# Optimization experiments

Hardware: AMD Instinct MI355X
Metric: run time of the kernel (lower is better)

The kernel has to match this reference:

```python
import jax, jax.numpy as jnp
import numpy as np

PS = 7  # window size
HEADS = 8


def setup_inputs() -> dict:
    key = jax.random.key(0)
    ks = jax.random.split(key, 5)
    b, C, H, W = 2, 384, 224, 224
    x = jax.random.normal(ks[0], (b, C, H, W), dtype=jnp.float32)
    # Conv2d(dim, 3*dim, k=1, bias=False) -> weight [3C, C]
    qkv_w = jax.random.normal(ks[1], (3 * C, C), dtype=jnp.float32) * (1.0 / np.sqrt(C))
    # depthwise Conv2d(3*dim, 3*dim, k=3, groups=3*dim) -> weight [3C, 1, 3, 3]
    dw_w = jax.random.normal(ks[2], (3 * C, 1, 3, 3), dtype=jnp.float32) * (1.0 / 3.0)
    # temperature parameter, initialized to ones like the module
    temperature = jnp.ones((HEADS, 1, 1), dtype=jnp.float32)
    # Conv2d(dim, dim, k=1, bias=False) -> weight [C, C]
    proj_w = jax.random.normal(ks[3], (C, C), dtype=jnp.float32) * (1.0 / np.sqrt(C))
    return {"x": x, "qkv_w": qkv_w, "dw_w": dw_w, "temperature": temperature, "proj_w": proj_w}


def _l2norm(t):
    n = jnp.sqrt(jnp.sum(t * t, axis=-1, keepdims=True))
    return t / jnp.maximum(n, 1e-12)  # matches F.normalize semantics


def reference(x, qkv_w, dw_w, temperature, proj_w):
    b, C, H, W = x.shape
    heads, ps = HEADS, PS
    d = C // heads
    nh, nw = H // ps, W // ps

    # 1x1 conv qkv projection (pointwise -> einsum)
    qkv = jnp.einsum('bchw,oc->bohw', x, qkv_w)
    # depthwise 3x3 conv, padding=1
    qkv = jax.lax.conv_general_dilated(
        qkv, dw_w, window_strides=(1, 1), padding='SAME',
        feature_group_count=3 * C, dimension_numbers=('NCHW', 'OIHW', 'NCHW'))
    q, k, v = jnp.split(qkv, 3, axis=1)

    def to_win(t):
        # b (head d) (nh ps) (nw ps) -> b (nh nw) head d (ps ps)
        t = t.reshape(b, heads, d, nh, ps, nw, ps)
        t = t.transpose(0, 3, 5, 1, 2, 4, 6)
        return t.reshape(b, nh * nw, heads, d, ps * ps)

    q, k, v = to_win(q), to_win(k), to_win(v)
    q = _l2norm(q)
    k = _l2norm(k)

    # channel-transposed attention: d x d scores per window
    attn = jnp.einsum('bwhds,bwhes->bwhde', q, k) * temperature
    attn = jax.nn.softmax(attn, axis=-1)
    out = jnp.einsum('bwhde,bwhes->bwhds', attn, v)

    # inverse rearrange: b (nh nw) head d (ps ps) -> b (head d) (nh ps) (nw ps)
    out = out.reshape(b, nh, nw, heads, d, ps, ps)
    out = out.transpose(0, 3, 4, 1, 5, 2, 6).reshape(b, C, H, W)

    return jnp.einsum('bchw,oc->bohw', out, proj_w)
```

## Files before the change

kernel.cpp:

```cpp
#include <hip/hip_runtime.h>


#define NB     2
#define CC     384
#define C3     1152
#define HH     224
#define WW2    224
#define HW     50176
#define NHEADS 8
#define DD     48
#define PSZ    7
#define NWINS  1024
#define SS     49
#define SSP    56
#define WSR    (NWINS*SSP)

typedef unsigned int  u32;
typedef unsigned short u16;
typedef __bf16 bf16x8 __attribute__((ext_vector_type(8)));
typedef float  f32x4  __attribute__((ext_vector_type(4)));

__device__ __forceinline__ u16 f2bf(float f){
  union { __bf16 h; u16 u; } v; v.h = (__bf16)f; return v.u;
}
__device__ __forceinline__ float bf2f(u16 h){
  union { u32 u; float f; } v; v.u = ((u32)h) << 16;
  return v.f;
}
__device__ __forceinline__ float u16lo(u32 u){
  union { u32 u; float f; } v; v.u = u << 16; return v.f;
}
__device__ __forceinline__ float u16hi(u32 u){
  union { u32 u; float f; } v; v.u = u & 0xffff0000u; return v.f;
}

typedef __attribute__((address_space(3))) u32 as3_u32;
typedef __attribute__((address_space(1))) const u32 as1_u32;
__device__ __forceinline__ void gld16(const void* g, void* l){
  __builtin_amdgcn_global_load_lds((as1_u32*)(unsigned long long)(g),
                                   (as3_u32*)(u32)(unsigned long long)(l),
                                   16, 0, 0);
}

__device__ __forceinline__ int xcdswz(int bid, int cpx){
  return (bid & 7)*cpx + (bid >> 3);
}

__device__ __forceinline__ int swz(int row, int col){
  return row*64 + (col ^ ((row & 7) << 3));
}

__global__ void k_cvt(const float* __restrict__ qw, const float* __restrict__ pw,
                      u16* __restrict__ qwb, u16* __restrict__ pwb){
  int i = blockIdx.x * 256 + threadIdx.x;
  if (i < C3*CC) qwb[i] = f2bf(qw[i]);
  if (i < CC*CC) pwb[i] = f2bf(pw[i]);
}

__global__ void k_sentinel(float* __restrict__ out, int n){
  int i = blockIdx.x * 256 + threadIdx.x;
  if (i < n) out[i] = 12345.0f;
}

#define CPAD 386
__global__ __launch_bounds__(256) void k_trx(const float* __restrict__ x,
                                             u16* __restrict__ xt){
  const int pt = blockIdx.x, b = blockIdx.y, tid = threadIdx.x;
  __shared__ u16 t[64*CPAD];
  const float* xb = x + (size_t)b*CC*HW + pt*64;
  #pragma unroll
  for (int it=0; it<24; ++it){
    int i = tid + it*256;
    int c = i >> 4, p4 = (i & 15)*4;
    float4 v = *(const float4*)(xb + (size_t)c*HW + p4);
    t[(p4+0)*CPAD + c] = f2bf(v.x);
    t[(p4+1)*CPAD + c] = f2bf(v.y);
    t[(p4+2)*CPAD + c] = f2bf(v.z);
    t[(p4+3)*CPAD + c] = f2bf(v.w);
  }
  __syncthreads();
  u32* dst = (u32*)(xt + ((size_t)b*HW + (size_t)pt*64)*CC);
  #pragma unroll
  for (int it=0; it<48; ++it){
    int j = tid + it*256;
    int p = j / 192, c2 = j - p*192;
    dst[j] = *(const u32*)(t + p*CPAD + c2*2);
  }
}

template<int OUT_F32, int MT, int CPX>
__global__ __launch_bounds__(256) void k_gemm(const u16* __restrict__ A,
    const u16* __restrict__ B, void* __restrict__ Cdst){
  __shared__ __align__(16) u16 As0[128*64], Bs0[128*64];
  __shared__ __align__(16) u16 As1[128*64], Bs1[128*64];
  const int wg = xcdswz(blockIdx.x, CPX);
  const int m0 = (wg % MT) * 128;
  const int t1 = wg / MT;
  const int n0 = (t1 % 392) * 128;
  const int b  = t1 / 392;
  const int M  = MT * 128;
  const int tid = threadIdx.x, lane = tid & 63, wv = tid >> 6;
  const int wm = (wv & 1) * 64, wn = (wv >> 1) * 64;
  const int lr = lane & 15, lg = lane >> 4;
  const u16* Bb = B + (size_t)b*HW*CC;

  f32x4 acc[4][4];
  #pragma unroll
  for (int i=0;i<4;++i)
    #pragma unroll
    for (int j=0;j<4;++j) acc[i][j] = {0.f,0.f,0.f,0.f};

  const int srow[4] = { (tid+  0)>>3, (tid+256)>>3, (tid+512)>>3, (tid+768)>>3 };
  const int sc8  = tid & 7;

  #define STAGE(AD, BD, K0) {                                             \
    _Pragma("unroll")                                                     \
    for (int i=0;i<4;++i){                                                \
      int row = srow[i];                                                  \
      int csrc = sc8 ^ (row & 7);                                         \
      gld16(A  + (size_t)(m0+row)*CC + (K0) + csrc*8, AD + (i*256+tid)*8);\
      gld16(Bb + (size_t)(n0+row)*CC + (K0) + csrc*8, BD + (i*256+tid)*8);\
    } }

  #define COMPUTE(AD, BD) {                                               \
    _Pragma("unroll")                                                     \
    for (int ks=0; ks<2; ++ks){                                           \
      const int cp = (((ks*4 + lg) ^ (lr & 7)) << 3);                     \
      bf16x8 af[4], bfr[4];                                               \
      _Pragma("unroll")                                                   \
      for (int i=0;i<4;++i) af[i]  = *(const bf16x8*)(AD + (wm + i*16 + lr)*64 + cp); \
      _Pragma("unroll")                                                   \
      for (int j=0;j<4;++j) bfr[j] = *(const bf16x8*)(BD + (wn + j*16 + lr)*64 + cp); \
      _Pragma("unroll")                                                   \
      for (int i=0;i<4;++i)                                               \
        _Pragma("unroll")                                                 \
        for (int j=0;j<4;++j)                                             \
          acc[i][j] = __builtin_amdgcn_mfma_f32_16x16x32_bf16(af[i], bfr[j], acc[i][j], 0, 0, 0); \
    } }

  STAGE(As0, Bs0, 0)
  __syncthreads();
  #pragma unroll
  for (int kk2=0; kk2<3; ++kk2){
    const int k0 = kk2*128;
    if (kk2*2+1 < 6) STAGE(As1, Bs1, k0+64)
    COMPUTE(As0, Bs0)
    __syncthreads();
    if (kk2*2+2 < 6) STAGE(As0, Bs0, k0+128)
    COMPUTE(As1, Bs1)
    __syncthreads();
  }
  #undef STAGE
  #undef COMPUTE

  #pragma unroll
  for (int i=0;i<4;++i){
    #pragma unroll
    for (int j=0;j<4;++j){
      const int row = m0 + wm + i*16 + lg*4;
      const int col = n0 + wn + j*16 + lr;
      if (OUT_F32){
        float* Cp = (float*)Cdst + (size_t)b*M*HW;
        #pragma unroll
        for (int r=0;r<4;++r) Cp[(size_t)(row+r)*HW + col] = acc[i][j][r];
      } else {
        u16* Cp = (u16*)Cdst + (size_t)b*M*HW;
        #pragma unroll
        for (int r=0;r<4;++r) Cp[(size_t)(row+r)*HW + col] = f2bf(acc[i][j][r]);
      }
    }
  }
}

#define DWL 240
__global__ __launch_bounds__(128) void k_dw(const u16* __restrict__ qkv,
    const float* __restrict__ dww, u16* __restrict__ qkv2){
  const int wg = xcdswz(blockIdx.x, 2304);
  const int wy = wg & 31;
  const int t1 = wg >> 5;
  const int o0 = (t1 % 288) * 4;
  const int b  = t1 / 288;
  const int tid = threadIdx.x;
  __shared__ __align__(16) u16 lin[4*9*DWL];

  const int y0 = wy*PSZ - 1;

  if (tid < 72){
    int ch = tid/18, rem = tid%18, r = rem>>1;
    lin[ch*9*DWL + r*DWL + ((rem&1) ? 232 : 7)] = 0;
  }

  #pragma unroll
  for (int it=0; it<8; ++it){
    int i = tid + it*128;
    if (i < 1008){
      int ch = i / 252, rem = i - ch*252;
      int r = rem / 28, c16 = rem - r*28;
      int y = y0 + r;
      uint4 v = {0,0,0,0};
      if (y >= 0 && y < HH)
        v = *(const uint4*)(qkv + (size_t)(b*C3 + o0 + ch)*HW + (size_t)y*WW2 + c16*8);
      *(uint4*)(lin + ch*9*DWL + r*DWL + 8 + c16*8) = v;
    }
  }
  __syncthreads();

  {
    const int ch = tid >> 5, wx = tid & 31;
    const u16* L = lin + ch*9*DWL;
    const int xb = wx*PSZ;
    const int s0 = (xb+7) & ~1;
    const bool par = (xb+7) & 1;

    float wk[9];
    #pragma unroll
    for (int i=0;i<9;++i) wk[i] = dww[(o0+ch)*9 + i];

    float tr[3][9];
    #define LOADROW(slot, r) {                                   \
      u32 u0 = *(const u32*)(L + (r)*DWL + s0);                  \
      u32 u1 = *(const u32*)(L + (r)*DWL + s0 + 2);              \
      u32 u2 = *(const u32*)(L + (r)*DWL + s0 + 4);              \
      u32 u3 = *(const u32*)(L + (r)*DWL + s0 + 6);              \
      u32 u4 = *(const u32*)(L + (r)*DWL + s0 + 8);              \
      float a0=u16lo(u0),a1=u16hi(u0),a2=u16lo(u1),a3=u16hi(u1); \
      float a4=u16lo(u2),a5=u16hi(u2),a6=u16lo(u3),a7=u16hi(u3); \
      float a8=u16lo(u4),a9=u16hi(u4);                           \
      tr[slot][0]=par?a1:a0; tr[slot][1]=par?a2:a1;              \
      tr[slot][2]=par?a3:a2; tr[slot][3]=par?a4:a3;              \
      tr[slot][4]=par?a5:a4; tr[slot][5]=par?a6:a5;              \
      tr[slot][6]=par?a7:a6; tr[slot][7]=par?a8:a7;              \
      tr[slot][8]=par?a9:a8; }

    LOADROW(0, 0)
    LOADROW(1, 1)

    u32 pk[28];
    pk[24] = 0; pk[25] = 0; pk[26] = 0; pk[27] = 0;
    #pragma unroll
    for (int pi=0; pi<7; ++pi){
      LOADROW((pi+2)%3, pi+2)
      const float* r0 = tr[pi%3];
      const float* r1 = tr[(pi+1)%3];
      const float* r2 = tr[(pi+2)%3];
      float o[7];
      #pragma unroll
      for (int pj=0; pj<7; ++pj){
        float s = 0.f;
        #pragma unroll
        for (int kx=0;kx<3;++kx){
          s += wk[kx]  *r0[pj+kx];
          s += wk[3+kx]*r1[pj+kx];
          s += wk[6+kx]*r2[pj+kx];
        }
        o[pj] = s;
      }
      #pragma unroll
      for (int pj=0; pj<7; ++pj){
        int idx = pi*7 + pj;
        u16 bv = f2bf(o[pj]);
        if ((idx & 1) == 0) pk[idx>>1] = (u32)bv;
        else                pk[idx>>1] |= ((u32)bv) << 16;
      }
    }
    u16* rec = qkv2 + ((size_t)(b*C3 + o0 + ch)*NWINS + (size_t)(wy*32 + wx))*SSP;
    #pragma unroll
    for (int i=0;i<7;++i) *(uint4*)(rec + i*8) = *(const uint4*)(pk + i*4);
  }
}

__global__ __launch_bounds__(256) void k_attn(const u16* __restrict__ qkv2,
    const float* __restrict__ temp, u16* __restrict__ aout){
  const int h = blockIdx.x, win = blockIdx.y, b = blockIdx.z;
  const int tid = threadIdx.x, lane = tid & 63, wv = tid >> 6;
  const int lr = lane & 15, lg = lane >> 4;

  __shared__ __align__(16) u16 q_s[48*64], k_s[48*64], v_t[64*64], p_s[48*64];
  __shared__ float invq[48], invk[48];

  for (int i=tid; i<48*32; i+=256){ ((u32*)q_s)[i]=0u; ((u32*)k_s)[i]=0u; ((u32*)p_s)[i]=0u; }
  for (int i=tid; i<64*32; i+=256) ((u32*)v_t)[i]=0u;
  __syncthreads();

  const u16* qsrc = qkv2 + ((size_t)(b*C3 +        h*DD)*NWINS + win)*SSP;
  const u16* ksrc = qkv2 + ((size_t)(b*C3 + CC   + h*DD)*NWINS + win)*SSP;
  const u16* vsrc = qkv2 + ((size_t)(b*C3 + 2*CC + h*DD)*NWINS + win)*SSP;
  for (int i=tid; i<48*25; i+=256){
    int dc = i / 25, c = i - dc*25;
    size_t off = (size_t)dc*WSR + 2*c;
    u32 vq = *(const u32*)(qsrc + off);
    u32 vk = *(const u32*)(ksrc + off);
    u32 vv = *(const u32*)(vsrc + off);
    int sw = swz(dc, 2*c);
    *(u32*)(q_s + sw) = vq;
    *(u32*)(k_s + sw) = vk;
    v_t[swz(2*c,   dc)] = (u16)(vv & 0xffffu);
    v_t[swz(2*c+1, dc)] = (u16)(vv >> 16);
  }
  __syncthreads();

  if (tid < 192){
    const int row96 = tid >> 1, half = tid & 1;
    const int rr = (row96 < 48) ? row96 : row96 - 48;
    const u16* a = (row96 < 48) ? q_s : k_s;
    const int s0 = half ? 25 : 0, s1 = half ? 49 : 25;
    float sum = 0.f;
    for (int s=s0; s<s1; ++s){ float v = bf2f(a[swz(rr,s)]); sum += v*v; }
    sum += __shfl_xor(sum, 1);
    if (!half){
      float inv = 1.f / fmaxf(sqrtf(sum), 1e-12f);
      if (row96 < 48) invq[rr] = inv * temp[h]; else invk[rr] = inv;
    }
  }
  __syncthreads();

  if (wv < 3){
    const int ti = wv;
    f32x4 c3[3];
    #pragma unroll
    for (int tj=0;tj<3;++tj) c3[tj] = {0.f,0.f,0.f,0.f};
    #pragma unroll
    for (int tj=0;tj<3;++tj){
      #pragma unroll
      for (int ks=0; ks<2; ++ks){
        bf16x8 a  = *(const bf16x8*)(q_s + swz(ti*16+lr, ks*32 + lg*8));
        bf16x8 bb = *(const bf16x8*)(k_s + swz(tj*16+lr, ks*32 + lg*8));
        c3[tj] = __builtin_amdgcn_mfma_f32_16x16x32_bf16(a, bb, c3[tj], 0,0,0);
      }
    }
    const float ik0 = invk[lr], ik1 = invk[16+lr], ik2 = invk[32+lr];
    #pragma unroll
    for (int r=0;r<4;++r){
      const int row = ti*16 + lg*4 + r;
      const float iq = invq[row];
      float l0 = c3[0][r]*iq*ik0, l1 = c3[1][r]*iq*ik1, l2 = c3[2][r]*iq*ik2;
      float m = fmaxf(fmaxf(l0,l1),l2);
      m = fmaxf(m, __shfl_xor(m,1)); m = fmaxf(m, __shfl_xor(m,2));
      m = fmaxf(m, __shfl_xor(m,4)); m = fmaxf(m, __shfl_xor(m,8));
      float e0 = __expf(l0-m), e1 = __expf(l1-m), e2 = __expf(l2-m);
      float s = e0+e1+e2;
      s += __shfl_xor(s,1); s += __shfl_xor(s,2);
      s += __shfl_xor(s,4); s += __shfl_xor(s,8);
      const float is = 1.f / s;
      p_s[swz(row, lr)]    = f2bf(e0*is);
      p_s[swz(row, 16+lr)] = f2bf(e1*is);
      p_s[swz(row, 32+lr)] = f2bf(e2*is);
    }
  }
  __syncthreads();

  const int wy = win >> 5, wx = win & 31;
  u16* ab = aout + (size_t)b*HW*CC + (size_t)h*DD;
  for (int t = wv; t < 12; t += 4){
    int ti = t >> 2, tj = t & 3;
    f32x4 c = {0.f,0.f,0.f,0.f};
    #pragma unroll
    for (int ks=0; ks<2; ++ks){
      bf16x8 a  = *(const bf16x8*)(p_s + swz(ti*16+lr, ks*32 + lg*8));
      bf16x8 bb = *(const bf16x8*)(v_t + swz(tj*16+lr, ks*32 + lg*8));
      c = __builtin_amdgcn_mfma_f32_16x16x32_bf16(a, bb, c, 0,0,0);
    }
    int scol = tj*16 + lr;
    if (scol < SS){
      int pi = scol / PSZ, pj = scol - pi*PSZ;
      size_t p = (size_t)(wy*PSZ + pi)*WW2 + wx*PSZ + pj;
      u32 lo = (u32)f2bf(c[0]) | ((u32)f2bf(c[1]) << 16);
      u32 hi = (u32)f2bf(c[2]) | ((u32)f2bf(c[3]) << 16);
      u32* dst = (u32*)(ab + p*CC + ti*16 + lg*4);
      dst[0] = lo; dst[1] = hi;
    }
  }
}

extern "C" void kernel_launch(void* const* d_in, const int* in_sizes, int n_in,
                              void* d_out, int out_size, void* d_ws, size_t ws_size,
                              hipStream_t stream) {
  const float* x     = (const float*)d_in[0];
  const float* qkvw  = (const float*)d_in[1];
  const float* dww   = (const float*)d_in[2];
  const float* temp  = (const float*)d_in[3];
  const float* projw = (const float*)d_in[4];
  float* out = (float*)d_out;

  const size_t SZ_QKV   = (size_t)NB*C3*HW*2;
  const size_t SZ_QKV2  = (size_t)NB*C3*NWINS*SSP*2;
  const size_t OFF_QKV2 = SZ_QKV;
  const size_t OFF_W1   = OFF_QKV2 + SZ_QKV2;
  const size_t OFF_W2   = OFF_W1 + (size_t)C3*CC*2;
  const size_t NEEDED   = OFF_W2 + (size_t)CC*CC*2;

  if (ws_size < NEEDED){
    k_sentinel<<<(out_size + 255)/256, 256, 0, stream>>>(out, out_size);
    return;
  }
  char* ws = (char*)d_ws;
  u16* qkv  = (u16*)ws;
  u16* qkv2 = (u16*)(ws + OFF_QKV2);
  u16* xt   = (u16*)(ws + OFF_QKV2);
  u16* ao   = (u16*)ws;
  u16* qwb  = (u16*)(ws + OFF_W1);
  u16* pwb  = (u16*)(ws + OFF_W2);

  k_cvt<<<dim3((C3*CC)/256), 256, 0, stream>>>(qkvw, projw, qwb, pwb);
  k_trx<<<dim3(784, NB), 256, 0, stream>>>(x, xt);
  k_gemm<0,9,882><<<dim3(7056), 256, 0, stream>>>(qwb, xt, qkv);
  k_dw<<<dim3(18432), 128, 0, stream>>>(qkv, dww, qkv2);
  k_attn<<<dim3(NHEADS, NWINS, NB), 256, 0, stream>>>(qkv2, temp, ao);
  k_gemm<1,3,294><<<dim3(2352), 256, 0, stream>>>(pwb, ao, out);
}
```

Before: 547.0 us.

## Process four heads per attention block with register-prefetched next-head loads

Each attention block now handles four heads of one window instead of one, and the block index is remapped through an XCD swizzle. The next head's q/k/v loads are issued into registers before the current head's compute and written to LDS afterwards, so global latency overlaps with MFMA work. MFMA sections are wrapped in s_setprio. This cuts launch count and per-block LDS zeroing, at the cost of more registers, less parallelism and extra barriers per block.

```diff
diff --git a/kernel.cpp b/kernel.cpp
--- a/kernel.cpp
+++ b/kernel.cpp
@@ -271,7 +271,10 @@
 
 __global__ __launch_bounds__(256) void k_attn(const u16* __restrict__ qkv2,
     const float* __restrict__ temp, u16* __restrict__ aout){
-  const int h = blockIdx.x, win = blockIdx.y, b = blockIdx.z;
+  const int wg  = xcdswz(blockIdx.x, 512);
+  const int hg  = wg & 1;
+  const int win = (wg >> 1) & 1023;
+  const int b   = wg >> 11;
   const int tid = threadIdx.x, lane = tid & 63, wv = tid >> 6;
   const int lr = lane & 15, lg = lane >> 4;
 
@@ -280,96 +283,130 @@
 
   for (int i=tid; i<48*32; i+=256){ ((u32*)q_s)[i]=0u; ((u32*)k_s)[i]=0u; ((u32*)p_s)[i]=0u; }
   for (int i=tid; i<64*32; i+=256) ((u32*)v_t)[i]=0u;
+
+  u32 off[16], lw[16]; bool val[16];
+  #pragma unroll
+  for (int j=0;j<16;++j){
+    int g = j*256 + tid;
+    val[j] = (g < 3600);
+    int t = (g >= 2400) ? 2 : ((g >= 1200) ? 1 : 0);
+    int gi = g - t*1200;
+    int dc = gi/25, c = gi - dc*25;
+    off[j] = (u32)((t*CC + dc)*WSR + 2*c);
+    lw[j]  = (u32)(dc | (c<<8) | (t<<16));
+  }
+
+  u32 ld[16];
+  #define ISSUE(HB) { _Pragma("unroll") \
+    for (int j=0;j<16;++j) if (val[j]) ld[j] = *(const u32*)((HB) + off[j]); }
+  #define WRITELDS() { _Pragma("unroll") \
+    for (int j=0;j<16;++j) if (val[j]) {                          \
+      int dc = lw[j] & 255, c = (lw[j]>>8) & 255;                 \
+      u32 t = lw[j]>>16;                                          \
+      if (t==0)      *(u32*)(q_s + swz(dc, 2*c)) = ld[j];         \
+      else if (t==1) *(u32*)(k_s + swz(dc, 2*c)) = ld[j];         \
+      else { v_t[swz(2*c,   dc)] = (u16)(ld[j] & 0xffffu);        \
+             v_t[swz(2*c+1, dc)] = (u16)(ld[j] >> 16); } } }
+
+  const u16* hb0 = qkv2 + ((size_t)(b*C3 + (hg*4)*DD)*NWINS + win)*SSP;
+  ISSUE(hb0)
   __syncthreads();
-
-  const u16* qsrc = qkv2 + ((size_t)(b*C3 +        h*DD)*NWINS + win)*SSP;
-  const u16* ksrc = qkv2 + ((size_t)(b*C3 + CC   + h*DD)*NWINS + win)*SSP;
-  const u16* vsrc = qkv2 + ((size_t)(b*C3 + 2*CC + h*DD)*NWINS + win)*SSP;
-  for (int i=tid; i<48*25; i+=256){
-    int dc = i / 25, c = i - dc*25;
-    size_t off = (size_t)dc*WSR + 2*c;
-    u32 vq = *(const u32*)(qsrc + off);
-    u32 vk = *(const u32*)(ksrc + off);
-    u32 vv = *(const u32*)(vsrc + off);
-    int sw = swz(dc, 2*c);
-    *(u32*)(q_s + sw) = vq;
-    *(u32*)(k_s + sw) = vk;
-    v_t[swz(2*c,   dc)] = (u16)(vv & 0xffffu);
-    v_t[swz(2*c+1, dc)] = (u16)(vv >> 16);
-  }
+  WRITELDS()
   __syncthreads();
 
-  if (tid < 192){
-    const int row96 = tid >> 1, half = tid & 1;
-    const int rr = (row96 < 48) ? row96 : row96 - 48;
-    const u16* a = (row96 < 48) ? q_s : k_s;
-    const int s0 = half ? 25 : 0, s1 = half ? 49 : 25;
-    float sum = 0.f;
-    for (int s=s0; s<s1; ++s){ float v = bf2f(a[swz(rr,s)]); sum += v*v; }
-    sum += __shfl_xor(sum, 1);
-    if (!half){
-      float inv = 1.f / fmaxf(sqrtf(sum), 1e-12f);
-      if (row96 < 48) invq[rr] = inv * temp[h]; else invk[rr] = inv;
-    }
-  }
-  __syncthreads();
-
-  if (wv < 3){
-    const int ti = wv;
-    f32x4 c3[3];
-    #pragma unroll
-    for (int tj=0;tj<3;++tj) c3[tj] = {0.f,0.f,0.f,0.f};
-    #pragma unroll
-    for (int tj=0;tj<3;++tj){
+  #pragma unroll
+  for (int hh=0; hh<4; ++hh){
+    const int h = hg*4 + hh;
+    if (hh < 3){
+      const u16* hbn = qkv2 + ((size_t)(b*C3 + (h+1)*DD)*NWINS + win)*SSP;
+      ISSUE(hbn)
+    }
+    if (tid < 192){
+      const int row96 = tid >> 1, half = tid & 1;
+      const int rr = (row96 < 48) ? row96 : row96 - 48;
+      const u16* a = (row96 < 48) ? q_s : k_s;
+      const int s0 = half ? 25 : 0, s1 = half ? 49 : 25;
+      float sum = 0.f;
+      for (int s=s0; s<s1; ++s){ float v = bf2f(a[swz(rr,s)]); sum += v*v; }
+      sum += __shfl_xor(sum, 1);
+      if (!half){
+        float inv = 1.f / fmaxf(sqrtf(sum), 1e-12f);
+        if (row96 < 48) invq[rr] = inv * temp[h]; else invk[rr] = inv;
+      }
+    }
+    __syncthreads();
+
+    if (wv < 3){
+      const int ti = wv;
+      f32x4 c3[3];
       #pragma unroll
-      for (int ks=0; ks<2; ++ks){
-        bf16x8 a  = *(const bf16x8*)(q_s + swz(ti*16+lr, ks*32 + lg*8));
-        bf16x8 bb = *(const bf16x8*)(k_s + swz(tj*16+lr, ks*32 + lg*8));
-        c3[tj] = __builtin_amdgcn_mfma_f32_16x16x32_bf16(a, bb, c3[tj], 0,0,0);
-      }
-    }
-    const float ik0 = invk[lr], ik1 = invk[16+lr], ik2 = invk[32+lr];
-    #pragma unroll
-    for (int r=0;r<4;++r){
-      const int row = ti*16 + lg*4 + r;
-      const float iq = invq[row];
-      float l0 = c3[0][r]*iq*ik0, l1 = c3[1][r]*iq*ik1, l2 = c3[2][r]*iq*ik2;
-      float m = fmaxf(fmaxf(l0,l1),l2);
-      m = fmaxf(m, __shfl_xor(m,1)); m = fmaxf(m, __shfl_xor(m,2));
-      m = fmaxf(m, __shfl_xor(m,4)); m = fmaxf(m, __shfl_xor(m,8));
-      float e0 = __expf(l0-m), e1 = __expf(l1-m), e2 = __expf(l2-m);
-      float s = e0+e1+e2;
-      s += __shfl_xor(s,1); s += __shfl_xor(s,2);
-      s += __shfl_xor(s,4); s += __shfl_xor(s,8);
-      const float is = 1.f / s;
-      p_s[swz(row, lr)]    = f2bf(e0*is);
-      p_s[swz(row, 16+lr)] = f2bf(e1*is);
-      p_s[swz(row, 32+lr)] = f2bf(e2*is);
-    }
-  }
-  __syncthreads();
-
-  const int wy = win >> 5, wx = win & 31;
-  u16* ab = aout + (size_t)b*HW*CC + (size_t)h*DD;
-  for (int t = wv; t < 12; t += 4){
-    int ti = t >> 2, tj = t & 3;
-    f32x4 c = {0.f,0.f,0.f,0.f};
-    #pragma unroll
-    for (int ks=0; ks<2; ++ks){
-      bf16x8 a  = *(const bf16x8*)(p_s + swz(ti*16+lr, ks*32 + lg*8));
-      bf16x8 bb = *(const bf16x8*)(v_t + swz(tj*16+lr, ks*32 + lg*8));
-      c = __builtin_amdgcn_mfma_f32_16x16x32_bf16(a, bb, c, 0,0,0);
-    }
-    int scol = tj*16 + lr;
-    if (scol < SS){
-      int pi = scol / PSZ, pj = scol - pi*PSZ;
-      size_t p = (size_t)(wy*PSZ + pi)*WW2 + wx*PSZ + pj;
-      u32 lo = (u32)f2bf(c[0]) | ((u32)f2bf(c[1]) << 16);
-      u32 hi = (u32)f2bf(c[2]) | ((u32)f2bf(c[3]) << 16);
-      u32* dst = (u32*)(ab + p*CC + ti*16 + lg*4);
-      dst[0] = lo; dst[1] = hi;
-    }
-  }
+      for (int tj=0;tj<3;++tj) c3[tj] = {0.f,0.f,0.f,0.f};
+      __builtin_amdgcn_s_setprio(1);
+      #pragma unroll
+      for (int tj=0;tj<3;++tj){
+        #pragma unroll
+        for (int ks=0; ks<2; ++ks){
+          bf16x8 a  = *(const bf16x8*)(q_s + swz(ti*16+lr, ks*32 + lg*8));
+          bf16x8 bb = *(const bf16x8*)(k_s + swz(tj*16+lr, ks*32 + lg*8));
+          c3[tj] = __builtin_amdgcn_mfma_f32_16x16x32_bf16(a, bb, c3[tj], 0,0,0);
+        }
+      }
+      __builtin_amdgcn_s_setprio(0);
+      const float ik0 = invk[lr], ik1 = invk[16+lr], ik2 = invk[32+lr];
+      #pragma unroll
+      for (int r=0;r<4;++r){
+        const int row = ti*16 + lg*4 + r;
+        const float iq = invq[row];
+        float l0 = c3[0][r]*iq*ik0, l1 = c3[1][r]*iq*ik1, l2 = c3[2][r]*iq*ik2;
+        float m = fmaxf(fmaxf(l0,l1),l2);
+        m = fmaxf(m, __shfl_xor(m,1)); m = fmaxf(m, __shfl_xor(m,2));
+        m = fmaxf(m, __shfl_xor(m,4)); m = fmaxf(m, __shfl_xor(m,8));
+        float e0 = __expf(l0-m), e1 = __expf(l1-m), e2 = __expf(l2-m);
+        float s = e0+e1+e2;
+        s += __shfl_xor(s,1); s += __shfl_xor(s,2);
+        s += __shfl_xor(s,4); s += __shfl_xor(s,8);
+        const float is = 1.f / s;
+        p_s[swz(row, lr)]    = f2bf(e0*is);
+        p_s[swz(row, 16+lr)] = f2bf(e1*is);
+        p_s[swz(row, 32+lr)] = f2bf(e2*is);
+      }
+    }
+    __syncthreads();
+
+    {
+      const int wy = win >> 5, wx = win & 31;
+      u16* ab = aout + (size_t)b*HW*CC + (size_t)h*DD;
+      for (int t = wv; t < 12; t += 4){
+        int ti = t >> 2, tj = t & 3;
+        f32x4 c = {0.f,0.f,0.f,0.f};
+        __builtin_amdgcn_s_setprio(1);
+        #pragma unroll
+        for (int ks=0; ks<2; ++ks){
+          bf16x8 a  = *(const bf16x8*)(p_s + swz(ti*16+lr, ks*32 + lg*8));
+          bf16x8 bb = *(const bf16x8*)(v_t + swz(tj*16+lr, ks*32 + lg*8));
+          c = __builtin_amdgcn_mfma_f32_16x16x32_bf16(a, bb, c, 0,0,0);
+        }
+        __builtin_amdgcn_s_setprio(0);
+        int scol = tj*16 + lr;
+        if (scol < SS){
+          int pi = scol / PSZ, pj = scol - pi*PSZ;
+          size_t p = (size_t)(wy*PSZ + pi)*WW2 + wx*PSZ + pj;
+          u32 lo = (u32)f2bf(c[0]) | ((u32)f2bf(c[1]) << 16);
+          u32 hi = (u32)f2bf(c[2]) | ((u32)f2bf(c[3]) << 16);
+          u32* dst = (u32*)(ab + p*CC + ti*16 + lg*4);
+          dst[0] = lo; dst[1] = hi;
+        }
+      }
+    }
+    __syncthreads();
+
+    if (hh < 3){
+      WRITELDS()
+      __syncthreads();
+    }
+  }
+  #undef ISSUE
+  #undef WRITELDS
 }
 
 extern "C" void kernel_launch(void* const* d_in, const int* in_sizes, int n_in,
@@ -405,6 +442,6 @@
   k_trx<<<dim3(784, NB), 256, 0, stream>>>(x, xt);
   k_gemm<0,9,882><<<dim3(7056), 256, 0, stream>>>(qwb, xt, qkv);
   k_dw<<<dim3(18432), 128, 0, stream>>>(qkv, dww, qkv2);
-  k_attn<<<dim3(NHEADS, NWINS, NB), 256, 0, stream>>>(qkv2, temp, ao);
+  k_attn<<<dim3(4096), 256, 0, stream>>>(qkv2, temp, ao);
   k_gemm<1,3,294><<<dim3(2352), 256, 0, stream>>>(pwb, ao, out);
 }
```

Result: slower. 576.6 us (+5.4%).

## Fuse depthwise conv into windowed attention kernel, dropping qkv2 intermediate

Applied to the files above, without the earlier changes.

The separate depthwise 3x3 kernel and attention kernel become one kernel. Each block loads a halo tile of the qkv projection for its (batch, head, window), runs the depthwise conv for the 144 q/k/v channels straight into shared memory, then performs normalization, softmax and the output MFMA. This removes the write and re-read of the windowed qkv2 buffer and one launch. In exchange each block does strided per-row global loads with halo overlap between neighbouring windows, and only 144 of 256 threads do the conv stage.

```diff
diff --git a/kernel.cpp b/kernel.cpp
--- a/kernel.cpp
+++ b/kernel.cpp
@@ -12,8 +12,6 @@
 #define PSZ    7
 #define NWINS  1024
 #define SS     49
-#define SSP    56
-#define WSR    (NWINS*SSP)
 
 typedef unsigned int  u32;
 typedef unsigned short u16;
@@ -172,78 +170,90 @@
   }
 }
 
-#define DWL 240
-__global__ __launch_bounds__(128) void k_dw(const u16* __restrict__ qkv,
-    const float* __restrict__ dww, u16* __restrict__ qkv2){
-  const int wg = xcdswz(blockIdx.x, 2304);
-  const int wy = wg & 31;
-  const int t1 = wg >> 5;
-  const int o0 = (t1 % 288) * 4;
-  const int b  = t1 / 288;
-  const int tid = threadIdx.x;
-  __shared__ __align__(16) u16 lin[4*9*DWL];
-
-  const int y0 = wy*PSZ - 1;
-
-  if (tid < 72){
-    int ch = tid/18, rem = tid%18, r = rem>>1;
-    lin[ch*9*DWL + r*DWL + ((rem&1) ? 232 : 7)] = 0;
-  }
-
-  #pragma unroll
-  for (int it=0; it<8; ++it){
-    int i = tid + it*128;
-    if (i < 1008){
-      int ch = i / 252, rem = i - ch*252;
-      int r = rem / 28, c16 = rem - r*28;
-      int y = y0 + r;
-      uint4 v = {0,0,0,0};
-      if (y >= 0 && y < HH)
-        v = *(const uint4*)(qkv + (size_t)(b*C3 + o0 + ch)*HW + (size_t)y*WW2 + c16*8);
-      *(uint4*)(lin + ch*9*DWL + r*DWL + 8 + c16*8) = v;
-    }
-  }
-  __syncthreads();
-
-  {
-    const int ch = tid >> 5, wx = tid & 31;
-    const u16* L = lin + ch*9*DWL;
-    const int xb = wx*PSZ;
-    const int s0 = (xb+7) & ~1;
-    const bool par = (xb+7) & 1;
+__global__ __launch_bounds__(256) void k_fattn(const u16* __restrict__ qkv,
+    const float* __restrict__ dww, const float* __restrict__ temp,
+    u16* __restrict__ aout){
+  const int wg  = xcdswz(blockIdx.x, 2048);
+  const int win = wg & 1023;
+  const int rest = wg >> 10;
+  const int h = rest & 7;
+  const int b = rest >> 3;
+  const int wy = win >> 5, wx = win & 31;
+  const int tid = threadIdx.x, lane = tid & 63, wv = tid >> 6;
+  const int lr = lane & 15, lg = lane >> 4;
+
+  __shared__ __align__(16) u16 xin[144*9*20];
+  __shared__ __align__(16) u16 q_s[48*64], k_s[48*64], v_t[64*64], p_s[48*64];
+  __shared__ float invq[48], invk[48];
+
+  const int xm1 = wx*PSZ - 1;
+  int a0 = xm1 & ~7; if (a0 < 0) a0 = 0;
+  const bool a0v = (a0 <= 208);
+
+  for (int i=tid; i<48*32; i+=256){ ((u32*)q_s)[i]=0u; ((u32*)k_s)[i]=0u; ((u32*)p_s)[i]=0u; }
+  for (int i=tid; i<64*32; i+=256) ((u32*)v_t)[i]=0u;
+
+  #pragma unroll
+  for (int j=0;j<6;++j){
+    int g = j*256 + tid;
+    if (g < 1296){
+      int ch = g / 9, row = g - ch*9;
+      int t  = ch / 48, d = ch - t*48;
+      int cmap = t*CC + h*DD + d;
+      int y = wy*PSZ - 1 + row;
+      bool yok = (y >= 0) & (y < HH);
+      uint4 v0 = {0,0,0,0}, v1 = {0,0,0,0};
+      if (yok){
+        const u16* src = qkv + ((size_t)(b*C3 + cmap))*HW + (size_t)y*WW2 + a0;
+        v0 = *(const uint4*)(src);
+        if (a0v) v1 = *(const uint4*)(src + 8);
+      }
+      u16* xr = xin + g*20;
+      *(u32*)(xr + 0)  = 0u;
+      *(u32*)(xr + 2)  = v0.x; *(u32*)(xr + 4)  = v0.y;
+      *(u32*)(xr + 6)  = v0.z; *(u32*)(xr + 8)  = v0.w;
+      *(u32*)(xr + 10) = v1.x; *(u32*)(xr + 12) = v1.y;
+      *(u32*)(xr + 14) = v1.z; *(u32*)(xr + 16) = v1.w;
+    }
+  }
+  __syncthreads();
+
+  if (tid < 144){
+    const int t = tid / 48, d = tid - t*48;
+    const int cmap = t*CC + h*DD + d;
+    const u16* X = xin + tid*9*20;
+    const int tb = xm1 - a0 + 2;
+    const int s0 = tb & ~1;
+    const bool par = tb & 1;
 
     float wk[9];
     #pragma unroll
-    for (int i=0;i<9;++i) wk[i] = dww[(o0+ch)*9 + i];
+    for (int i=0;i<9;++i) wk[i] = dww[cmap*9 + i];
 
     float tr[3][9];
     #define LOADROW(slot, r) {                                   \
-      u32 u0 = *(const u32*)(L + (r)*DWL + s0);                  \
-      u32 u1 = *(const u32*)(L + (r)*DWL + s0 + 2);              \
-      u32 u2 = *(const u32*)(L + (r)*DWL + s0 + 4);              \
-      u32 u3 = *(const u32*)(L + (r)*DWL + s0 + 6);              \
-      u32 u4 = *(const u32*)(L + (r)*DWL + s0 + 8);              \
-      float a0=u16lo(u0),a1=u16hi(u0),a2=u16lo(u1),a3=u16hi(u1); \
-      float a4=u16lo(u2),a5=u16hi(u2),a6=u16lo(u3),a7=u16hi(u3); \
-      float a8=u16lo(u4),a9=u16hi(u4);                           \
-      tr[slot][0]=par?a1:a0; tr[slot][1]=par?a2:a1;              \
-      tr[slot][2]=par?a3:a2; tr[slot][3]=par?a4:a3;              \
-      tr[slot][4]=par?a5:a4; tr[slot][5]=par?a6:a5;              \
-      tr[slot][6]=par?a7:a6; tr[slot][7]=par?a8:a7;              \
-      tr[slot][8]=par?a9:a8; }
+      u32 u0 = *(const u32*)(X + (r)*20 + s0);                   \
+      u32 u1 = *(const u32*)(X + (r)*20 + s0 + 2);               \
+      u32 u2 = *(const u32*)(X + (r)*20 + s0 + 4);               \
+      u32 u3 = *(const u32*)(X + (r)*20 + s0 + 6);               \
+      u32 u4 = *(const u32*)(X + (r)*20 + s0 + 8);               \
+      float a0_=u16lo(u0),a1_=u16hi(u0),a2_=u16lo(u1),a3_=u16hi(u1); \
+      float a4_=u16lo(u2),a5_=u16hi(u2),a6_=u16lo(u3),a7_=u16hi(u3); \
+      float a8_=u16lo(u4),a9_=u16hi(u4);                         \
+      tr[slot][0]=par?a1_:a0_; tr[slot][1]=par?a2_:a1_;          \
+      tr[slot][2]=par?a3_:a2_; tr[slot][3]=par?a4_:a3_;          \
+      tr[slot][4]=par?a5_:a4_; tr[slot][5]=par?a6_:a5_;          \
+      tr[slot][6]=par?a7_:a6_; tr[slot][7]=par?a8_:a7_;          \
+      tr[slot][8]=par?a9_:a8_; }
 
     LOADROW(0, 0)
     LOADROW(1, 1)
-
-    u32 pk[28];
-    pk[24] = 0; pk[25] = 0; pk[26] = 0; pk[27] = 0;
     #pragma unroll
     for (int pi=0; pi<7; ++pi){
       LOADROW((pi+2)%3, pi+2)
       const float* r0 = tr[pi%3];
       const float* r1 = tr[(pi+1)%3];
       const float* r2 = tr[(pi+2)%3];
-      float o[7];
       #pragma unroll
       for (int pj=0; pj<7; ++pj){
         float s = 0.f;
@@ -253,49 +263,14 @@
           s += wk[3+kx]*r1[pj+kx];
           s += wk[6+kx]*r2[pj+kx];
         }
-        o[pj] = s;
-      }
-      #pragma unroll
-      for (int pj=0; pj<7; ++pj){
-        int idx = pi*7 + pj;
-        u16 bv = f2bf(o[pj]);
-        if ((idx & 1) == 0) pk[idx>>1] = (u32)bv;
-        else                pk[idx>>1] |= ((u32)bv) << 16;
-      }
-    }
-    u16* rec = qkv2 + ((size_t)(b*C3 + o0 + ch)*NWINS + (size_t)(wy*32 + wx))*SSP;
-    #pragma unroll
-    for (int i=0;i<7;++i) *(uint4*)(rec + i*8) = *(const uint4*)(pk + i*4);
-  }
-}
-
-__global__ __launch_bounds__(256) void k_attn(const u16* __restrict__ qkv2,
-    const float* __restrict__ temp, u16* __restrict__ aout){
-  const int h = blockIdx.x, win = blockIdx.y, b = blockIdx.z;
-  const int tid = threadIdx.x, lane = tid & 63, wv = tid >> 6;
-  const int lr = lane & 15, lg = lane >> 4;
-
-  __shared__ __align__(16) u16 q_s[48*64], k_s[48*64], v_t[64*64], p_s[48*64];
-  __shared__ float invq[48], invk[48];
-
-  for (int i=tid; i<48*32; i+=256){ ((u32*)q_s)[i]=0u; ((u32*)k_s)[i]=0u; ((u32*)p_s)[i]=0u; }
-  for (int i=tid; i<64*32; i+=256) ((u32*)v_t)[i]=0u;
-  __syncthreads();
-
-  const u16* qsrc = qkv2 + ((size_t)(b*C3 +        h*DD)*NWINS + win)*SSP;
-  const u16* ksrc = qkv2 + ((size_t)(b*C3 + CC   + h*DD)*NWINS + win)*SSP;
-  const u16* vsrc = qkv2 + ((size_t)(b*C3 + 2*CC + h*DD)*NWINS + win)*SSP;
-  for (int i=tid; i<48*25; i+=256){
-    int dc = i / 25, c = i - dc*25;
-    size_t off = (size_t)dc*WSR + 2*c;
-    u32 vq = *(const u32*)(qsrc + off);
-    u32 vk = *(const u32*)(ksrc + off);
-    u32 vv = *(const u32*)(vsrc + off);
-    int sw = swz(dc, 2*c);
-    *(u32*)(q_s + sw) = vq;
-    *(u32*)(k_s + sw) = vk;
-    v_t[swz(2*c,   dc)] = (u16)(vv & 0xffffu);
-    v_t[swz(2*c+1, dc)] = (u16)(vv >> 16);
+        u16 bv = f2bf(s);
+        int px = pi*7 + pj;
+        if (t == 0)      q_s[swz(d, px)] = bv;
+        else if (t == 1) k_s[swz(d, px)] = bv;
+        else             v_t[swz(px, d)] = bv;
+      }
+    }
+    #undef LOADROW
   }
   __syncthreads();
 
@@ -303,9 +278,9 @@
     const int row96 = tid >> 1, half = tid & 1;
     const int rr = (row96 < 48) ? row96 : row96 - 48;
     const u16* a = (row96 < 48) ? q_s : k_s;
-    const int s0 = half ? 25 : 0, s1 = half ? 49 : 25;
+    const int s0n = half ? 25 : 0, s1n = half ? 49 : 25;
     float sum = 0.f;
-    for (int s=s0; s<s1; ++s){ float v = bf2f(a[swz(rr,s)]); sum += v*v; }
+    for (int s=s0n; s<s1n; ++s){ float v = bf2f(a[swz(rr,s)]); sum += v*v; }
     sum += __shfl_xor(sum, 1);
     if (!half){
       float inv = 1.f / fmaxf(sqrtf(sum), 1e-12f);
@@ -349,25 +324,26 @@
   }
   __syncthreads();
 
-  const int wy = win >> 5, wx = win & 31;
-  u16* ab = aout + (size_t)b*HW*CC + (size_t)h*DD;
-  for (int t = wv; t < 12; t += 4){
-    int ti = t >> 2, tj = t & 3;
-    f32x4 c = {0.f,0.f,0.f,0.f};
-    #pragma unroll
-    for (int ks=0; ks<2; ++ks){
-      bf16x8 a  = *(const bf16x8*)(p_s + swz(ti*16+lr, ks*32 + lg*8));
-      bf16x8 bb = *(const bf16x8*)(v_t + swz(tj*16+lr, ks*32 + lg*8));
-      c = __builtin_amdgcn_mfma_f32_16x16x32_bf16(a, bb, c, 0,0,0);
-    }
-    int scol = tj*16 + lr;
-    if (scol < SS){
-      int pi = scol / PSZ, pj = scol - pi*PSZ;
-      size_t p = (size_t)(wy*PSZ + pi)*WW2 + wx*PSZ + pj;
-      u32 lo = (u32)f2bf(c[0]) | ((u32)f2bf(c[1]) << 16);
-      u32 hi = (u32)f2bf(c[2]) | ((u32)f2bf(c[3]) << 16);
-      u32* dst = (u32*)(ab + p*CC + ti*16 + lg*4);
-      dst[0] = lo; dst[1] = hi;
+  {
+    u16* ab = aout + (size_t)b*HW*CC + (size_t)h*DD;
+    for (int t = wv; t < 12; t += 4){
+      int ti = t >> 2, tj = t & 3;
+      f32x4 c = {0.f,0.f,0.f,0.f};
+      #pragma unroll
+      for (int ks=0; ks<2; ++ks){
+        bf16x8 a  = *(const bf16x8*)(p_s + swz(ti*16+lr, ks*32 + lg*8));
+        bf16x8 bb = *(const bf16x8*)(v_t + swz(tj*16+lr, ks*32 + lg*8));
+        c = __builtin_amdgcn_mfma_f32_16x16x32_bf16(a, bb, c, 0,0,0);
+      }
+      int scol = tj*16 + lr;
+      if (scol < SS){
+        int pi = scol / PSZ, pj = scol - pi*PSZ;
+        size_t p = (size_t)(wy*PSZ + pi)*WW2 + wx*PSZ + pj;
+        u32 lo = (u32)f2bf(c[0]) | ((u32)f2bf(c[1]) << 16);
+        u32 hi = (u32)f2bf(c[2]) | ((u32)f2bf(c[3]) << 16);
+        u32* dst = (u32*)(ab + p*CC + ti*16 + lg*4);
+        dst[0] = lo; dst[1] = hi;
+      }
     }
   }
 }
@@ -382,29 +358,27 @@
   const float* projw = (const float*)d_in[4];
   float* out = (float*)d_out;
 
-  const size_t SZ_QKV   = (size_t)NB*C3*HW*2;
-  const size_t SZ_QKV2  = (size_t)NB*C3*NWINS*SSP*2;
-  const size_t OFF_QKV2 = SZ_QKV;
-  const size_t OFF_W1   = OFF_QKV2 + SZ_QKV2;
-  const size_t OFF_W2   = OFF_W1 + (size_t)C3*CC*2;
-  const size_t NEEDED   = OFF_W2 + (size_t)CC*CC*2;
+  const size_t SZ_QKV = (size_t)NB*C3*HW*2;
+  const size_t SZ_XT  = (size_t)NB*HW*CC*2;
+  const size_t OFF_XT = SZ_QKV;
+  const size_t OFF_W1 = OFF_XT + SZ_XT;
+  const size_t OFF_W2 = OFF_W1 + (size_t)C3*CC*2;
+  const size_t NEEDED = OFF_W2 + (size_t)CC*CC*2;
 
   if (ws_size < NEEDED){
     k_sentinel<<<(out_size + 255)/256, 256, 0, stream>>>(out, out_size);
     return;
   }
   char* ws = (char*)d_ws;
-  u16* qkv  = (u16*)ws;
-  u16* qkv2 = (u16*)(ws + OFF_QKV2);
-  u16* xt   = (u16*)(ws + OFF_QKV2);
-  u16* ao   = (u16*)ws;
-  u16* qwb  = (u16*)(ws + OFF_W1);
-  u16* pwb  = (u16*)(ws + OFF_W2);
+  u16* qkv = (u16*)ws;
+  u16* xt  = (u16*)(ws + OFF_XT);
+  u16* ao  = (u16*)(ws + OFF_XT);
+  u16* qwb = (u16*)(ws + OFF_W1);
+  u16* pwb = (u16*)(ws + OFF_W2);
 
   k_cvt<<<dim3((C3*CC)/256), 256, 0, stream>>>(qkvw, projw, qwb, pwb);
   k_trx<<<dim3(784, NB), 256, 0, stream>>>(x, xt);
   k_gemm<0,9,882><<<dim3(7056), 256, 0, stream>>>(qwb, xt, qkv);
-  k_dw<<<dim3(18432), 128, 0, stream>>>(qkv, dww, qkv2);
-  k_attn<<<dim3(NHEADS, NWINS, NB), 256, 0, stream>>>(qkv2, temp, ao);
+  k_fattn<<<dim3(16384), 256, 0, stream>>>(qkv, dww, temp, ao);
   k_gemm<1,3,294><<<dim3(2352), 256, 0, stream>>>(pwb, ao, out);
 }
```

New measurement: 642.1 us. 17.4% more time.
